# Kernel optimization log

Measured on AMD Instinct MI355X. Metric: run time of the kernel, lower is better.

## Reference

```python
import jax, jax.numpy as jnp
import numpy as np

B, L, DIN = 2, 4096, 1024
W = 64            # windowsize
G, H = 8, 8       # groups, heads per group
DQ = DV = 64
FF = 1024
NEG = -1e30


def rmsnorm(x, gamma, d):
    # F.normalize(x, dim=-1) * sqrt(d) * gamma
    n = jnp.sqrt(jnp.sum(x * x, axis=-1, keepdims=True))
    return x / jnp.maximum(n, 1e-12) * (d ** 0.5) * gamma


def setup_inputs() -> dict:
    key = jax.random.key(0)
    ks = jax.random.split(key, 8)
    s = 0.02
    return {
        "x": jax.random.normal(ks[0], (B, L, DIN), jnp.float32),
        "norm_gamma": jnp.ones((DIN,), jnp.float32),
        "Wq_w": jax.random.normal(ks[1], (G * H * DQ, DIN), jnp.float32) * s,
        "Wq_b": jnp.zeros((G * H * DQ,), jnp.float32),
        "Wkv_w": jax.random.normal(ks[2], (G * (DQ + DV), DIN), jnp.float32) * s,
        "Wkv_b": jnp.zeros((G * (DQ + DV),), jnp.float32),
        "wz_gamma1": jnp.ones((G * H * DV,), jnp.float32),
        "W1_w": jax.random.normal(ks[3], (2 * FF, G * H * DV), jnp.float32) * s,
        "W1_b": jnp.zeros((2 * FF,), jnp.float32),
        "wz_gamma2": jnp.ones((2 * FF,), jnp.float32),
        "W2_w": jax.random.normal(ks[4], (FF, 2 * FF), jnp.float32) * s,
        "W2_b": jnp.zeros((FF,), jnp.float32),
    }


def reference(x, norm_gamma, Wq_w, Wq_b, Wkv_w, Wkv_b,
              wz_gamma1, W1_w, W1_b, wz_gamma2, W2_w, W2_b):
    w2, w4 = W // 2, W // 4
    S = 2 * L // W  # number of query chunks (L % W == 0 -> drop_last path)

    xn = rmsnorm(x, norm_gamma, DIN)
    q = xn @ Wq_w.T + Wq_b          # [B, L, G*H*DQ]
    kv = xn @ Wkv_w.T + Wkv_b       # [B, L, G*(DQ+DV)]

    # pad_to_multiple(kv, W, mod=W//2): L % W == 0 -> append W//2 zeros
    kv = jnp.pad(kv, ((0, 0), (0, w2), (0, 0)))
    k, v = jnp.split(kv, 2, axis=-1)  # each [B, L+W/2, G*DQ]
    # F.pad W//4 both sides, then overlapping windows of size W, stride W//2
    k = jnp.pad(k, ((0, 0), (w4, w4), (0, 0)))  # [B, L+W, G*DQ]
    v = jnp.pad(v, ((0, 0), (w4, w4), (0, 0)))
    idx = jnp.arange(S)[:, None] * w2 + jnp.arange(W)[None, :]  # [S, W] (drop_last applied)
    kwin = k[:, idx].reshape(B, S, W, G, DQ).transpose(0, 3, 1, 2, 4)  # [B,G,S,W,DQ]
    vwin = v[:, idx].reshape(B, S, W, G, DV).transpose(0, 3, 1, 2, 4)  # [B,G,S,W,DV]

    # 'B (S w) (G H D) -> B G H S w D'
    qh = q.reshape(B, S, w2, G, H, DQ).transpose(0, 3, 4, 1, 2, 5)  # [B,G,H,S,w2,DQ]

    qk = jnp.einsum('bghsqd,bgskd->bghsqk', qh, kwin) * (1.0 / DQ ** 0.5)
    # edge masking: first chunk can't see left pad, last chunk can't see right pad
    maskb = jnp.zeros((S, W), bool).at[0, :w4].set(True).at[S - 1, W - w4:].set(True)
    qk = jnp.where(maskb[None, None, None, :, None, :], NEG, qk)
    attn = jax.nn.softmax(qk, axis=-1)
    o = jnp.einsum('bghsqk,bgskd->bghsqd', attn, vwin)
    o = o.transpose(0, 3, 4, 1, 2, 5).reshape(B, L, G * H * DV)  # 'B G H S w D -> B (S w) (G H D)'

    # Wz: RMSNorm -> Linear -> SiLU -> RMSNorm -> Linear -> SiLU (dropout=0)
    z = rmsnorm(o, wz_gamma1, G * H * DV)
    z = jax.nn.silu(z @ W1_w.T + W1_b)
    z = rmsnorm(z, wz_gamma2, 2 * FF)
    z = jax.nn.silu(z @ W2_w.T + W2_b)
    return z
```

## Files before the change

### kernel.cpp

```cpp
#include <hip/hip_runtime.h>
#include <cstdint>

typedef _Float16 f16;
typedef f16 f16x4 __attribute__((ext_vector_type(4)));
typedef f16 f16x8 __attribute__((ext_vector_type(8)));
typedef float f32x4 __attribute__((ext_vector_type(4)));

#define MFMA16(a, b, c) __builtin_amdgcn_mfma_f32_16x16x32_f16(a, b, c, 0, 0, 0)

static __device__ __forceinline__ void gload16(const void* g, void* l) {
    __builtin_amdgcn_global_load_lds(
        (const __attribute__((address_space(1))) uint32_t*)g,
        (__attribute__((address_space(3))) uint32_t*)l, 16, 0, 0);
}

static __device__ __forceinline__ float blockReduceSum256(float v) {
    __shared__ float red[4];
#pragma unroll
    for (int off = 32; off > 0; off >>= 1) v += __shfl_xor(v, off);
    if ((threadIdx.x & 63) == 0) red[threadIdx.x >> 6] = v;
    __syncthreads();
    return red[0] + red[1] + red[2] + red[3];
}

__global__ __launch_bounds__(256) void k_rmsnorm_x(const float* __restrict__ x,
                                                   const float* __restrict__ gamma,
                                                   f16* __restrict__ out) {
    size_t row = blockIdx.x;
    const float4 v = reinterpret_cast<const float4*>(x + row * 1024)[threadIdx.x];
    float ss = v.x * v.x + v.y * v.y + v.z * v.z + v.w * v.w;
    ss = blockReduceSum256(ss);
    float sc = 32.0f / fmaxf(sqrtf(ss), 1e-12f);
    const float4 g = reinterpret_cast<const float4*>(gamma)[threadIdx.x];
    f16x4 o;
    o[0] = (f16)(v.x * sc * g.x); o[1] = (f16)(v.y * sc * g.y);
    o[2] = (f16)(v.z * sc * g.z); o[3] = (f16)(v.w * sc * g.w);
    *reinterpret_cast<f16x4*>(out + row * 1024 + threadIdx.x * 4) = o;
}

template <int D>
__global__ __launch_bounds__(256) void k_rowss(const f16* __restrict__ in,
                                               float* __restrict__ sc) {
    constexpr int PER = D / 256;
    size_t row = blockIdx.x;
    const f16* ir = in + row * D;
    int c0 = threadIdx.x * PER;
    float ss = 0.f;
#pragma unroll
    for (int i = 0; i < PER; i += 8) {
        f16x8 h = *reinterpret_cast<const f16x8*>(ir + c0 + i);
#pragma unroll
        for (int e = 0; e < 8; ++e) { float f = (float)h[e]; ss += f * f; }
    }
    ss = blockReduceSum256(ss);
    if (threadIdx.x == 0)
        sc[row] = sqrtf((float)D) / fmaxf(sqrtf(ss), 1e-12f);
}

__global__ __launch_bounds__(256) void k_cast(const float* __restrict__ in,
                                              f16* __restrict__ out, int n4) {
    int i = blockIdx.x * 256 + threadIdx.x;
    if (i >= n4) return;
    float4 v = reinterpret_cast<const float4*>(in)[i];
    f16x4 o; o[0] = (f16)v.x; o[1] = (f16)v.y; o[2] = (f16)v.z; o[3] = (f16)v.w;
    *reinterpret_cast<f16x4*>(out + (size_t)i * 4) = o;
}

__global__ __launch_bounds__(256) void k_cast_g(const float* __restrict__ in,
                                                f16* __restrict__ out,
                                                const float* __restrict__ gamma,
                                                int kmask, int n4) {
    int i = blockIdx.x * 256 + threadIdx.x;
    if (i >= n4) return;
    float4 v = reinterpret_cast<const float4*>(in)[i];
    int e0 = (i * 4) & kmask;
    f16x4 o;
    o[0] = (f16)(v.x * gamma[e0]); o[1] = (f16)(v.y * gamma[e0 + 1]);
    o[2] = (f16)(v.z * gamma[e0 + 2]); o[3] = (f16)(v.w * gamma[e0 + 3]);
    *reinterpret_cast<f16x4*>(out + (size_t)i * 4) = o;
}

__global__ __launch_bounds__(256) void k_bias_cat(const float* __restrict__ a,
                                                  const float* __restrict__ b,
                                                  float* __restrict__ o) {
    int i = blockIdx.x * 256 + threadIdx.x;
    o[i] = (i < 4096) ? a[i] : b[i - 4096];
}

template <int BN, int EPI, int MODE>
__global__ __launch_bounds__(512, 2) void k_gemm8p(const f16* __restrict__ A,
                                                   const f16* __restrict__ Bt,
                                                   const float* __restrict__ bias,
                                                   const float* __restrict__ rowsc,
                                                   void* __restrict__ Cout,
                                                   int M, int N, int K) {
    constexpr int BM = 256;
    constexpr int WN = BN / 64, WM = 8 / WN, WR = BM / WM;
    constexpr int MW = WR / 16, MH = MW / 2;
    constexpr int LA = 2, LB = BN / 128;
    constexpr int WFULL = 2 * (LA + LB), WHALF = LA + LB;
    constexpr int AK = BM * 32;
    constexpr int BKE = BN * 32;
    constexpr int SE = 2 * AK + 2 * BKE;

    __shared__ alignas(16) f16 lds[2 * SE];

    const int nb = N / BN;
    int bn, bm;
    if (MODE == 0) { bn = blockIdx.x & 7; bm = blockIdx.x >> 3; }
    else           { bn = blockIdx.x % nb; bm = blockIdx.x / nb; }

    const int tid = threadIdx.x, w = tid >> 6, l = tid & 63;
    const int wm = w / WN, wn = w % WN;
    const int lrow = l & 15, lq = l >> 4;
    const int g = (lrow >> 1) & 3;

    const f16* Ab = A + (size_t)bm * BM * K;
    const f16* Bb = Bt + (size_t)bn * BN * K;
    const int NT = K >> 6;

    int aoff[MW], boff[4];
#pragma unroll
    for (int m = 0; m < MW; ++m)
        aoff[m] = (wm * WR + m * 16 + lrow) * 32 + 8 * (lq ^ g);
#pragma unroll
    for (int n = 0; n < 4; ++n)
        boff[n] = (wn * 64 + n * 16 + lrow) * 32 + 8 * (lq ^ g);

    auto stageA = [&](int k0, f16* region) {
#pragma unroll
        for (int q = 0; q < LA; ++q) {
            int r = q * 128 + w * 16 + (l >> 2);
            int c = 8 * ((l & 3) ^ ((r >> 1) & 3));
            gload16(Ab + (size_t)r * K + k0 + c, region + q * 4096 + w * 512);
        }
    };
    auto stageB = [&](int k0, f16* region) {
#pragma unroll
        for (int q = 0; q < LB; ++q) {
            int r = q * 128 + w * 16 + (l >> 2);
            int c = 8 * ((l & 3) ^ ((r >> 1) & 3));
            gload16(Bb + (size_t)r * K + k0 + c, region + q * 4096 + w * 512);
        }
    };
    auto rdA = [&](f16x8* d, const f16* base, int h) {
#pragma unroll
        for (int m = 0; m < MH; ++m)
            d[m] = *reinterpret_cast<const f16x8*>(base + aoff[h * MH + m]);
    };
    auto rdB = [&](f16x8* d, const f16* base) {
#pragma unroll
        for (int n = 0; n < 4; ++n)
            d[n] = *reinterpret_cast<const f16x8*>(base + boff[n]);
    };

    f32x4 acc[MW][4] = {};
    f16x8 afA[MH], afB[MH], bfA[4], bfB[4];

    stageA(0, lds);
    stageB(0, lds + 2 * AK);
    stageA(32, lds + AK);
    stageB(32, lds + 2 * AK + BKE);
    stageA(64, lds + SE);
    stageB(64, lds + SE + 2 * AK);
    asm volatile("s_waitcnt vmcnt(%0)" :: "i"(WFULL) : "memory");
    __builtin_amdgcn_s_barrier();
    rdA(afA, lds, 0);
    rdB(bfA, lds + 2 * AK);
    __builtin_amdgcn_sched_barrier(0);

    for (int t = 0; t < NT; ++t) {
        f16* sc_ = lds + (t & 1) * SE;
        f16* sn_ = lds + ((t & 1) ^ 1) * SE;

        __builtin_amdgcn_s_barrier();
        __builtin_amdgcn_s_setprio(1);
#pragma unroll
        for (int m = 0; m < MH; ++m)
#pragma unroll
            for (int n = 0; n < 4; ++n)
                acc[m][n] = MFMA16(afA[m], bfA[n], acc[m][n]);
        __builtin_amdgcn_s_setprio(0);
        if (t + 1 < NT) stageA((t + 1) * 64 + 32, sn_ + AK);
        rdA(afB, sc_, 1);
        __builtin_amdgcn_sched_barrier(0);

        __builtin_amdgcn_s_barrier();
        __builtin_amdgcn_s_setprio(1);
#pragma unroll
        for (int m = 0; m < MH; ++m)
#pragma unroll
            for (int n = 0; n < 4; ++n)
                acc[MH + m][n] = MFMA16(afB[m], bfA[n], acc[MH + m][n]);
        __builtin_amdgcn_s_setprio(0);
        if (t + 1 < NT) stageB((t + 1) * 64 + 32, sn_ + 2 * AK + BKE);
        if (t < NT - 1) asm volatile("s_waitcnt vmcnt(%0)" :: "i"(WFULL) : "memory");
        else            asm volatile("s_waitcnt vmcnt(0)" ::: "memory");
        __builtin_amdgcn_s_barrier();
        rdA(afA, sc_ + AK, 0);
        rdB(bfB, sc_ + 2 * AK + BKE);
        __builtin_amdgcn_sched_barrier(0);

        __builtin_amdgcn_s_barrier();
        __builtin_amdgcn_s_setprio(1);
#pragma unroll
        for (int m = 0; m < MH; ++m)
#pragma unroll
            for (int n = 0; n < 4; ++n)
                acc[m][n] = MFMA16(afA[m], bfB[n], acc[m][n]);
        __builtin_amdgcn_s_setprio(0);
        if (t + 2 < NT) stageA((t + 2) * 64, sc_);
        rdA(afB, sc_ + AK, 1);
        __builtin_amdgcn_sched_barrier(0);

        __builtin_amdgcn_s_barrier();
        __builtin_amdgcn_s_setprio(1);
#pragma unroll
        for (int m = 0; m < MH; ++m)
#pragma unroll
            for (int n = 0; n < 4; ++n)
                acc[MH + m][n] = MFMA16(afB[m], bfB[n], acc[MH + m][n]);
        __builtin_amdgcn_s_setprio(0);
        if (t + 2 < NT) stageB((t + 2) * 64, sc_ + 2 * AK);
        if (t + 1 < NT) {
            if (t < NT - 2) asm volatile("s_waitcnt vmcnt(%0)" :: "i"(WFULL) : "memory");
            else            asm volatile("s_waitcnt vmcnt(%0)" :: "i"(WHALF) : "memory");
            __builtin_amdgcn_s_barrier();
            rdA(afA, sn_, 0);
            rdB(bfA, sn_ + 2 * AK);
            __builtin_amdgcn_sched_barrier(0);
        }
    }

    const size_t row0 = (size_t)bm * BM + wm * WR;
    const int col0 = bn * BN + wn * 64;
    float bsv[4];
#pragma unroll
    for (int n = 0; n < 4; ++n) bsv[n] = bias[col0 + n * 16 + lrow];
#pragma unroll
    for (int m = 0; m < MW; ++m) {
#pragma unroll
        for (int r = 0; r < 4; ++r) {
            const size_t row = row0 + m * 16 + lq * 4 + r;
            float scl = (EPI >= 1) ? rowsc[row] : 1.0f;
#pragma unroll
            for (int n = 0; n < 4; ++n) {
                float v = acc[m][n][r];
                if (EPI >= 1) v = v * scl;
                v += bsv[n];
                if (EPI >= 1) v = v / (1.f + __expf(-v));
                const size_t idx = row * N + col0 + n * 16 + lrow;
                if (EPI == 2) reinterpret_cast<float*>(Cout)[idx] = v;
                else          reinterpret_cast<f16*>(Cout)[idx] = (f16)v;
            }
        }
    }
}

__global__ __launch_bounds__(256) void k_attn(const f16* __restrict__ qkv,
                                              f16* __restrict__ o) {
    __shared__ alignas(16) f16 Ksm[64 * 64];
    __shared__ alignas(16) f16 Vtsm[64 * 64];
    __shared__ alignas(16) f16 Psm[4][64 * 64];
    const int idx = blockIdx.x;
    const int s = idx & 127;
    const int g = (idx >> 7) & 7;
    const int b = idx >> 10;
    const int tid = threadIdx.x;
    const int w = tid >> 6, l = tid & 63;

    const int baseR = s * 32 - 16;
#pragma unroll
    for (int i = 0; i < 2; ++i) {
        const int j = i * 32 + (tid >> 3);
        const int d0 = (tid & 7) * 8;
        const int R = baseR + j;
        f16x8 kvv = {}, vvv = {};
        if (R >= 0 && R < 4096) {
            const f16* rp = qkv + ((size_t)(b * 4096 + R)) * 5120 + 4096 + g * 64 + d0;
            kvv = *reinterpret_cast<const f16x8*>(rp);
            vvv = *reinterpret_cast<const f16x8*>(rp + 512);
        }
        *reinterpret_cast<f16x8*>(&Ksm[j * 64 + d0]) = kvv;
#pragma unroll
        for (int e = 0; e < 8; ++e) Vtsm[(d0 + e) * 64 + j] = vvv[e];
    }

    const int lrow = l & 15, lk = (l >> 4) * 8;
    f16x8 aq[4][2];
#pragma unroll
    for (int m = 0; m < 4; ++m) {
        const int qr = w * 64 + m * 16 + lrow;
        const int h = qr >> 5, qi = qr & 31;
        const f16* qp = qkv + ((size_t)(b * 4096 + s * 32 + qi)) * 5120 + (g * 8 + h) * 64 + lk;
        aq[m][0] = *reinterpret_cast<const f16x8*>(qp);
        aq[m][1] = *reinterpret_cast<const f16x8*>(qp + 32);
    }
    __syncthreads();

    f32x4 acc[4][4] = {};
#pragma unroll
    for (int kk = 0; kk < 2; ++kk) {
        f16x8 bk[4];
#pragma unroll
        for (int n = 0; n < 4; ++n)
            bk[n] = *reinterpret_cast<const f16x8*>(&Ksm[(n * 16 + lrow) * 64 + kk * 32 + lk]);
#pragma unroll
        for (int m = 0; m < 4; ++m)
#pragma unroll
            for (int n = 0; n < 4; ++n)
                acc[m][n] = MFMA16(aq[m][kk], bk[n], acc[m][n]);
    }

    const int nlo = (s == 0) ? 1 : 0;
    const int nhi = (s == 127) ? 3 : 4;
#pragma unroll
    for (int m = 0; m < 4; ++m) {
#pragma unroll
        for (int r = 0; r < 4; ++r) {
            float xv[4];
#pragma unroll
            for (int n = 0; n < 4; ++n) xv[n] = acc[m][n][r] * 0.125f;
            float mx = -1e30f;
            for (int n = nlo; n < nhi; ++n) mx = fmaxf(mx, xv[n]);
#pragma unroll
            for (int off = 8; off > 0; off >>= 1) mx = fmaxf(mx, __shfl_xor(mx, off));
            float pv[4]; float sum = 0.f;
#pragma unroll
            for (int n = 0; n < 4; ++n) {
                float e = (n >= nlo && n < nhi) ? __expf(xv[n] - mx) : 0.f;
                pv[n] = e; sum += e;
            }
#pragma unroll
            for (int off = 8; off > 0; off >>= 1) sum += __shfl_xor(sum, off);
            const float inv = 1.f / sum;
            const int prow = m * 16 + (l >> 4) * 4 + r;
#pragma unroll
            for (int n = 0; n < 4; ++n)
                Psm[w][prow * 64 + n * 16 + lrow] = (f16)(pv[n] * inv);
        }
    }
    __syncthreads();

    f32x4 oacc[4][4] = {};
#pragma unroll
    for (int kk = 0; kk < 2; ++kk) {
        f16x8 ap[4], bv[4];
#pragma unroll
        for (int m = 0; m < 4; ++m)
            ap[m] = *reinterpret_cast<const f16x8*>(&Psm[w][(m * 16 + lrow) * 64 + kk * 32 + lk]);
#pragma unroll
        for (int n = 0; n < 4; ++n)
            bv[n] = *reinterpret_cast<const f16x8*>(&Vtsm[(n * 16 + lrow) * 64 + kk * 32 + lk]);
#pragma unroll
        for (int m = 0; m < 4; ++m)
#pragma unroll
            for (int n = 0; n < 4; ++n)
                oacc[m][n] = MFMA16(ap[m], bv[n], oacc[m][n]);
    }
    const int lr4 = (l >> 4) * 4;
#pragma unroll
    for (int m = 0; m < 4; ++m) {
#pragma unroll
        for (int r = 0; r < 4; ++r) {
            const int qr = w * 64 + m * 16 + lr4 + r;
            const int h = qr >> 5, qi = qr & 31;
            f16* op = o + ((size_t)(b * 4096 + s * 32 + qi)) * 4096 + (g * 8 + h) * 64;
#pragma unroll
            for (int n = 0; n < 4; ++n) op[n * 16 + lrow] = (f16)oacc[m][n][r];
        }
    }
}

extern "C" void kernel_launch(void* const* d_in, const int* in_sizes, int n_in,
                              void* d_out, int out_size, void* d_ws, size_t ws_size,
                              hipStream_t stream) {
    const float* x     = (const float*)d_in[0];
    const float* ng    = (const float*)d_in[1];
    const float* Wq_w  = (const float*)d_in[2];
    const float* Wq_b  = (const float*)d_in[3];
    const float* Wkv_w = (const float*)d_in[4];
    const float* Wkv_b = (const float*)d_in[5];
    const float* g1    = (const float*)d_in[6];
    const float* W1_w  = (const float*)d_in[7];
    const float* W1_b  = (const float*)d_in[8];
    const float* g2    = (const float*)d_in[9];
    const float* W2_w  = (const float*)d_in[10];
    const float* W2_b  = (const float*)d_in[11];
    float* out = (float*)d_out;

    char* p = (char*)d_ws;
    f16* qkv  = (f16*)(p);
    f16* h1   = (f16*)(p);
    f16* xn   = (f16*)(p + 83886080);
    f16* ob   = (f16*)(p + 83886080);
    f16* w1   = (f16*)(p + 150994944);
    f16* w2   = (f16*)(p + 167772160);
    f16* wqkv = (f16*)(p + 171966464);
    float* cb  = (float*)(p + 182452224);
    float* sc1 = (float*)(p + 182472704);
    float* sc2 = (float*)(p + 182505472);

    k_cast<<<4096, 256, 0, stream>>>(Wq_w, wqkv, 4096 * 1024 / 4);
    k_cast<<<1024, 256, 0, stream>>>(Wkv_w, wqkv + 4096 * 1024, 1024 * 1024 / 4);
    k_cast_g<<<8192, 256, 0, stream>>>(W1_w, w1, g1, 4095, 2048 * 4096 / 4);
    k_cast_g<<<2048, 256, 0, stream>>>(W2_w, w2, g2, 2047, 1024 * 2048 / 4);
    k_bias_cat<<<20, 256, 0, stream>>>(Wq_b, Wkv_b, cb);
    k_rmsnorm_x<<<8192, 256, 0, stream>>>(x, ng, xn);

    k_gemm8p<256, 0, 1><<<640, 512, 0, stream>>>(xn, wqkv, cb, nullptr, qkv, 8192, 5120, 1024);

    k_attn<<<2048, 256, 0, stream>>>(qkv, ob);

    k_rowss<4096><<<8192, 256, 0, stream>>>(ob, sc1);
    k_gemm8p<256, 1, 0><<<256, 512, 0, stream>>>(ob, w1, W1_b, sc1, h1, 8192, 2048, 4096);
    k_rowss<2048><<<8192, 256, 0, stream>>>(h1, sc2);
    k_gemm8p<128, 2, 0><<<256, 512, 0, stream>>>(h1, w2, W2_b, sc2, (void*)out, 8192, 1024, 2048);

    (void)in_sizes; (void)n_in; (void)out_size; (void)ws_size;
}
```

Before: 394.5 us.

## Interleave GEMM MFMAs with LDS reads and global loads via sched_group_barrier

Restructures the GEMM main loop so that global-to-LDS staging and LDS fragment reads are issued before each MFMA block. It uses sched_group_barrier to interleave the MFMAs with the DS reads and VMEM loads, instead of running them as separate serialized phases. The loop is peeled into a steady-state loop plus two tail iterations, which removes the per-iteration conditionals. The setprio hints are dropped and the vmcnt wait points move to new positions. The aim is to hide LDS and global latency behind MFMA work, at the risk of a subtle error in the vmcnt counts or buffer reuse.

```diff
diff --git a/kernel.cpp b/kernel.cpp
--- a/kernel.cpp
+++ b/kernel.cpp
@@ -12,6 +12,19 @@
     __builtin_amdgcn_global_load_lds(
         (const __attribute__((address_space(1))) uint32_t*)g,
         (__attribute__((address_space(3))) uint32_t*)l, 16, 0, 0);
+}
+
+template <int NM, int ND, int NV>
+static __device__ __forceinline__ void sgb_phase() {
+    if (NV > 0) __builtin_amdgcn_sched_group_barrier(0x10, NV, 0);
+    constexpr int PER = NM / ND;
+#pragma unroll
+    for (int i = 0; i < ND; ++i) {
+        __builtin_amdgcn_sched_group_barrier(0x8, PER, 0);
+        __builtin_amdgcn_sched_group_barrier(0x100, 1, 0);
+    }
+    if (NM - PER * ND > 0)
+        __builtin_amdgcn_sched_group_barrier(0x8, NM - PER * ND, 0);
 }
 
 static __device__ __forceinline__ float blockReduceSum256(float v) {
@@ -98,7 +111,7 @@
     constexpr int WN = BN / 64, WM = 8 / WN, WR = BM / WM;
     constexpr int MW = WR / 16, MH = MW / 2;
     constexpr int LA = 2, LB = BN / 128;
-    constexpr int WFULL = 2 * (LA + LB), WHALF = LA + LB;
+    constexpr int VS = 2 * LA + LB;
     constexpr int AK = BM * 32;
     constexpr int BKE = BN * 32;
     constexpr int SE = 2 * AK + 2 * BKE;
@@ -143,12 +156,12 @@
             gload16(Bb + (size_t)r * K + k0 + c, region + q * 4096 + w * 512);
         }
     };
-    auto rdA = [&](f16x8* d, const f16* base, int h) {
+    auto rdA = [&](f16x8 (&d)[MH], const f16* base, int h) {
 #pragma unroll
         for (int m = 0; m < MH; ++m)
             d[m] = *reinterpret_cast<const f16x8*>(base + aoff[h * MH + m]);
     };
-    auto rdB = [&](f16x8* d, const f16* base) {
+    auto rdB = [&](f16x8 (&d)[4], const f16* base) {
 #pragma unroll
         for (int n = 0; n < 4; ++n)
             d[n] = *reinterpret_cast<const f16x8*>(base + boff[n]);
@@ -157,79 +170,105 @@
     f32x4 acc[MW][4] = {};
     f16x8 afA[MH], afB[MH], bfA[4], bfB[4];
 
-    stageA(0, lds);
-    stageB(0, lds + 2 * AK);
-    stageA(32, lds + AK);
-    stageB(32, lds + 2 * AK + BKE);
-    stageA(64, lds + SE);
-    stageB(64, lds + SE + 2 * AK);
-    asm volatile("s_waitcnt vmcnt(%0)" :: "i"(WFULL) : "memory");
+    auto mfmaLo = [&](f16x8 (&af)[MH], f16x8 (&bf)[4]) {
+#pragma unroll
+        for (int m = 0; m < MH; ++m)
+#pragma unroll
+            for (int n = 0; n < 4; ++n)
+                acc[m][n] = MFMA16(af[m], bf[n], acc[m][n]);
+    };
+    auto mfmaHi = [&](f16x8 (&af)[MH], f16x8 (&bf)[4]) {
+#pragma unroll
+        for (int m = 0; m < MH; ++m)
+#pragma unroll
+            for (int n = 0; n < 4; ++n)
+                acc[MH + m][n] = MFMA16(af[m], bf[n], acc[MH + m][n]);
+    };
+
+    stageA(0, lds);             stageB(0, lds + 2 * AK);
+    stageA(32, lds + AK);       stageB(32, lds + 2 * AK + BKE);
+    stageA(64, lds + SE);       stageB(64, lds + SE + 2 * AK);
+    asm volatile("s_waitcnt vmcnt(%0)" :: "i"(2 * (LA + LB)) : "memory");
     __builtin_amdgcn_s_barrier();
     rdA(afA, lds, 0);
     rdB(bfA, lds + 2 * AK);
-    __builtin_amdgcn_sched_barrier(0);
-
-    for (int t = 0; t < NT; ++t) {
-        f16* sc_ = lds + (t & 1) * SE;
-        f16* sn_ = lds + ((t & 1) ^ 1) * SE;
-
-        __builtin_amdgcn_s_barrier();
-        __builtin_amdgcn_s_setprio(1);
-#pragma unroll
-        for (int m = 0; m < MH; ++m)
-#pragma unroll
-            for (int n = 0; n < 4; ++n)
-                acc[m][n] = MFMA16(afA[m], bfA[n], acc[m][n]);
-        __builtin_amdgcn_s_setprio(0);
-        if (t + 1 < NT) stageA((t + 1) * 64 + 32, sn_ + AK);
-        rdA(afB, sc_, 1);
-        __builtin_amdgcn_sched_barrier(0);
-
-        __builtin_amdgcn_s_barrier();
-        __builtin_amdgcn_s_setprio(1);
-#pragma unroll
-        for (int m = 0; m < MH; ++m)
-#pragma unroll
-            for (int n = 0; n < 4; ++n)
-                acc[MH + m][n] = MFMA16(afB[m], bfA[n], acc[MH + m][n]);
-        __builtin_amdgcn_s_setprio(0);
-        if (t + 1 < NT) stageB((t + 1) * 64 + 32, sn_ + 2 * AK + BKE);
-        if (t < NT - 1) asm volatile("s_waitcnt vmcnt(%0)" :: "i"(WFULL) : "memory");
-        else            asm volatile("s_waitcnt vmcnt(0)" ::: "memory");
-        __builtin_amdgcn_s_barrier();
-        rdA(afA, sc_ + AK, 0);
-        rdB(bfB, sc_ + 2 * AK + BKE);
-        __builtin_amdgcn_sched_barrier(0);
-
-        __builtin_amdgcn_s_barrier();
-        __builtin_amdgcn_s_setprio(1);
-#pragma unroll
-        for (int m = 0; m < MH; ++m)
-#pragma unroll
-            for (int n = 0; n < 4; ++n)
-                acc[m][n] = MFMA16(afA[m], bfB[n], acc[m][n]);
-        __builtin_amdgcn_s_setprio(0);
-        if (t + 2 < NT) stageA((t + 2) * 64, sc_);
-        rdA(afB, sc_ + AK, 1);
-        __builtin_amdgcn_sched_barrier(0);
-
-        __builtin_amdgcn_s_barrier();
-        __builtin_amdgcn_s_setprio(1);
-#pragma unroll
-        for (int m = 0; m < MH; ++m)
-#pragma unroll
-            for (int n = 0; n < 4; ++n)
-                acc[MH + m][n] = MFMA16(afB[m], bfB[n], acc[MH + m][n]);
-        __builtin_amdgcn_s_setprio(0);
-        if (t + 2 < NT) stageB((t + 2) * 64, sc_ + 2 * AK);
-        if (t + 1 < NT) {
-            if (t < NT - 2) asm volatile("s_waitcnt vmcnt(%0)" :: "i"(WFULL) : "memory");
-            else            asm volatile("s_waitcnt vmcnt(%0)" :: "i"(WHALF) : "memory");
-            __builtin_amdgcn_s_barrier();
-            rdA(afA, sn_, 0);
-            rdB(bfA, sn_ + 2 * AK);
-            __builtin_amdgcn_sched_barrier(0);
-        }
+
+    const int NTm2 = NT - 2;
+    for (int t = 0; t < NTm2; ++t) {
+        f16* s0 = lds + (t & 1) * SE;
+        f16* s1 = lds + ((t & 1) ^ 1) * SE;
+        const int kn1 = (t + 1) << 6;
+        const int kn2 = (t + 2) << 6;
+        __builtin_amdgcn_s_barrier();
+        stageA(kn1 + 32, s1 + AK);
+        rdA(afB, s0, 1);
+        mfmaLo(afA, bfA);
+        sgb_phase<MH * 4, MH, LA>();
+        asm volatile("s_waitcnt vmcnt(%0)" :: "i"(VS) : "memory");
+        __builtin_amdgcn_s_barrier();
+        stageB(kn1 + 32, s1 + 2 * AK + BKE);
+        rdA(afA, s0 + AK, 0);
+        rdB(bfB, s0 + 2 * AK + BKE);
+        mfmaHi(afB, bfA);
+        sgb_phase<MH * 4, MH + 4, LB>();
+        __builtin_amdgcn_s_barrier();
+        stageA(kn2, s0);
+        rdA(afB, s0 + AK, 1);
+        mfmaLo(afA, bfB);
+        sgb_phase<MH * 4, MH, LA>();
+        asm volatile("s_waitcnt vmcnt(%0)" :: "i"(VS) : "memory");
+        __builtin_amdgcn_s_barrier();
+        stageB(kn2, s0 + 2 * AK);
+        rdA(afA, s1, 0);
+        rdB(bfA, s1 + 2 * AK);
+        mfmaHi(afB, bfB);
+        sgb_phase<MH * 4, MH + 4, LB>();
+    }
+    {
+        const int t = NTm2;
+        f16* s0 = lds + (t & 1) * SE;
+        f16* s1 = lds + ((t & 1) ^ 1) * SE;
+        const int kn1 = (t + 1) << 6;
+        __builtin_amdgcn_s_barrier();
+        stageA(kn1 + 32, s1 + AK);
+        rdA(afB, s0, 1);
+        mfmaLo(afA, bfA);
+        sgb_phase<MH * 4, MH, LA>();
+        asm volatile("s_waitcnt vmcnt(%0)" :: "i"(VS) : "memory");
+        __builtin_amdgcn_s_barrier();
+        stageB(kn1 + 32, s1 + 2 * AK + BKE);
+        rdA(afA, s0 + AK, 0);
+        rdB(bfB, s0 + 2 * AK + BKE);
+        mfmaHi(afB, bfA);
+        sgb_phase<MH * 4, MH + 4, LB>();
+        __builtin_amdgcn_s_barrier();
+        rdA(afB, s0 + AK, 1);
+        mfmaLo(afA, bfB);
+        sgb_phase<MH * 4, MH, 0>();
+        asm volatile("s_waitcnt vmcnt(%0)" :: "i"(LA + LB) : "memory");
+        __builtin_amdgcn_s_barrier();
+        rdA(afA, s1, 0);
+        rdB(bfA, s1 + 2 * AK);
+        mfmaHi(afB, bfB);
+        sgb_phase<MH * 4, MH + 4, 0>();
+    }
+    {
+        f16* s0 = lds + ((NT - 1) & 1) * SE;
+        __builtin_amdgcn_s_barrier();
+        rdA(afB, s0, 1);
+        mfmaLo(afA, bfA);
+        sgb_phase<MH * 4, MH, 0>();
+        asm volatile("s_waitcnt vmcnt(0)" ::: "memory");
+        __builtin_amdgcn_s_barrier();
+        rdA(afA, s0 + AK, 0);
+        rdB(bfB, s0 + 2 * AK + BKE);
+        mfmaHi(afB, bfA);
+        sgb_phase<MH * 4, MH + 4, 0>();
+        __builtin_amdgcn_s_barrier();
+        rdA(afB, s0 + AK, 1);
+        mfmaLo(afA, bfB);
+        sgb_phase<MH * 4, MH, 0>();
+        mfmaHi(afB, bfB);
     }
 
     const size_t row0 = (size_t)bm * BM + wm * WR;
```

Result: faster. 371.9 us (-5.7%).
